# Kernel tuning notes

Measured on AMD Instinct MI355X. Metric: run time of the kernel, lower is better.

The kernel has to match this reference:

```python
import jax, jax.numpy as jnp
import numpy as np

IN, H1, H2, H3, H4, OUT = 512, 2048, 2048, 1024, 512, 1


def setup_inputs() -> dict:
    key = jax.random.key(0)
    ks = jax.random.split(key, 12)
    def lin(k, fan_in, fan_out):
        # torch Linear default init: U(-1/sqrt(fan_in), 1/sqrt(fan_in))
        bound = 1.0 / np.sqrt(fan_in)
        k1, k2 = jax.random.split(k)
        W = jax.random.uniform(k1, (fan_out, fan_in), jnp.float32, -bound, bound)
        b = jax.random.uniform(k2, (fan_out,), jnp.float32, -bound, bound)
        return W, b
    x = jax.random.normal(ks[0], (16384, IN), jnp.float32)
    cross_w = jnp.ones((IN,), jnp.float32)   # init.constant_(1.0)
    cross_b = jnp.zeros((IN,), jnp.float32)  # init.constant_(0.0)
    W1, b1 = lin(ks[1], IN, H1)
    W2, b2 = lin(ks[2], H1, H2)
    W3, b3 = lin(ks[3], H2, H3)
    W4, b4 = lin(ks[4], H3, H4)
    Wo, bo = lin(ks[5], H4, OUT)
    return {"x": x, "cross_w": cross_w, "cross_b": cross_b,
            "W1": W1, "b1": b1, "W2": W2, "b2": b2,
            "W3": W3, "b3": b3, "W4": W4, "b4": b4,
            "Wo": Wo, "bo": bo}


def reference(x, cross_w, cross_b, W1, b1, W2, b2, W3, b3, W4, b4, Wo, bo):
    # Cross layer: bmm(x0[...,None], x[...,None,:]) . w == x0 * (x . w)
    # (mathematically identical, avoids the O(f^2) outer product)
    xw = x @ cross_w                         # [B]
    h = x * xw[:, None] + cross_b + x        # [B, IN]
    h = jax.nn.relu(h @ W1.T + b1)           # [B, H1]
    h = jax.nn.relu(h @ W2.T + b2)           # [B, H2]
    h = jax.nn.relu(h @ W3.T + b3)           # [B, H3]
    h = jax.nn.relu(h @ W4.T + b4)           # [B, H4]
    return h @ Wo.T + bo                     # [B, OUT]
```

## Files before the change

kernel.cpp:

```cpp
#include <hip/hip_runtime.h>


#define BK 64

typedef __bf16 bf16x8 __attribute__((ext_vector_type(8)));
typedef float  f32x4  __attribute__((ext_vector_type(4)));
typedef unsigned short u16x4 __attribute__((ext_vector_type(4)));

__device__ __forceinline__ unsigned short f2bf(float f) {
    unsigned int u = __builtin_bit_cast(unsigned int, f);
    u += 0x7fffu + ((u >> 16) & 1u);
    return (unsigned short)(u >> 16);
}

__device__ __forceinline__ void async16(const void* g, void* l) {
    __builtin_amdgcn_global_load_lds(
        (const __attribute__((address_space(1))) unsigned int*)g,
        (__attribute__((address_space(3))) unsigned int*)l,
        16, 0, 0);
}

template<int BN>
__global__ __launch_bounds__(256, 2)
void gemm_bt_bias_relu(const unsigned short* __restrict__ A,
                       const unsigned short* __restrict__ B,
                       const float* __restrict__ bias,
                       unsigned short* __restrict__ C,
                       int M, int N, int K)
{
    constexpr int JT = BN / 32;
    __shared__ __align__(16) unsigned short As[128 * BK];
    __shared__ __align__(16) unsigned short Bs[BN * BK];

    const int tid  = threadIdx.x;
    const int lane = tid & 63;
    const int wave = tid >> 6;
    const int quad = lane >> 4;
    const int l16  = lane & 15;

    const int bm = blockIdx.x * 128;
    const int bn = blockIdx.y * BN;
    const int wm = (wave & 1) * 64;
    const int wn = (wave >> 1) * (BN / 2);

    const int lrow = tid >> 3;
    const int gcol = ((tid & 7) ^ (lrow & 7)) * 8;

    const unsigned short* gaBase = A + (size_t)(bm + lrow) * K + gcol;
    const unsigned short* gbBase = B + (size_t)(bn + lrow) * K + gcol;

    unsigned short* lA = As + tid * 8;
    unsigned short* lB = Bs + tid * 8;

    const int xa = l16 & 7;
    const unsigned short* As_w = As + (wm + l16) * BK;
    const unsigned short* Bs_w = Bs + (wn + l16) * BK;
    const int c0 = (quad ^ xa) * 8;
    const int c1 = ((quad ^ 4) ^ xa) * 8;

    f32x4 acc[4][JT] = {};

    for (int k0 = 0; k0 < K; k0 += BK) {
#pragma unroll
        for (int i = 0; i < 4; ++i)
            async16(gaBase + (size_t)(i * 32) * K + k0, lA + i * 2048);
#pragma unroll
        for (int i = 0; i < JT; ++i)
            async16(gbBase + (size_t)(i * 32) * K + k0, lB + i * 2048);
        __syncthreads();

#pragma unroll
        for (int kk = 0; kk < 2; ++kk) {
            const int cs = kk ? c1 : c0;
            bf16x8 af[4], bfr[JT];
#pragma unroll
            for (int i = 0; i < 4; ++i)  af[i]  = *(const bf16x8*)(As_w + i * 16 * BK + cs);
#pragma unroll
            for (int j = 0; j < JT; ++j) bfr[j] = *(const bf16x8*)(Bs_w + j * 16 * BK + cs);
#pragma unroll
            for (int i = 0; i < 4; ++i)
#pragma unroll
                for (int j = 0; j < JT; ++j)
                    acc[i][j] = __builtin_amdgcn_mfma_f32_16x16x32_bf16(
                        af[i], bfr[j], acc[i][j], 0, 0, 0);
        }
        __syncthreads();
    }

    float bv[JT];
#pragma unroll
    for (int j = 0; j < JT; ++j) bv[j] = bias[bn + wn + j * 16 + l16];

#pragma unroll
    for (int i = 0; i < 4; ++i) {
        const int row0 = bm + wm + i * 16 + quad * 4;
#pragma unroll
        for (int j = 0; j < JT; ++j) {
            const int col = bn + wn + j * 16 + l16;
#pragma unroll
            for (int r = 0; r < 4; ++r) {
                float v = acc[i][j][r] + bv[j];
                v = fmaxf(v, 0.0f);
                C[(size_t)(row0 + r) * N + col] = f2bf(v);
            }
        }
    }
}

__global__ __launch_bounds__(256, 2)
void gemm_bt_head(const unsigned short* __restrict__ A,
                  const unsigned short* __restrict__ B,
                  const float* __restrict__ bias,
                  const float* __restrict__ Wo,
                  float* __restrict__ out,
                  int M, int N, int K)
{
    constexpr int BN = 128;
    constexpr int JT = 4;
    __shared__ __align__(16) unsigned short As[128 * BK];
    __shared__ __align__(16) unsigned short Bs[BN * BK];

    const int tid  = threadIdx.x;
    const int lane = tid & 63;
    const int wave = tid >> 6;
    const int quad = lane >> 4;
    const int l16  = lane & 15;

    const int bm = blockIdx.x * 128;
    const int bn = blockIdx.y * BN;
    const int wm = (wave & 1) * 64;
    const int wn = (wave >> 1) * 64;

    const int lrow = tid >> 3;
    const int gcol = ((tid & 7) ^ (lrow & 7)) * 8;

    const unsigned short* gaBase = A + (size_t)(bm + lrow) * K + gcol;
    const unsigned short* gbBase = B + (size_t)(bn + lrow) * K + gcol;

    unsigned short* lA = As + tid * 8;
    unsigned short* lB = Bs + tid * 8;

    const int xa = l16 & 7;
    const unsigned short* As_w = As + (wm + l16) * BK;
    const unsigned short* Bs_w = Bs + (wn + l16) * BK;
    const int c0 = (quad ^ xa) * 8;
    const int c1 = ((quad ^ 4) ^ xa) * 8;

    f32x4 acc[4][JT] = {};

    for (int k0 = 0; k0 < K; k0 += BK) {
#pragma unroll
        for (int i = 0; i < 4; ++i)
            async16(gaBase + (size_t)(i * 32) * K + k0, lA + i * 2048);
#pragma unroll
        for (int i = 0; i < JT; ++i)
            async16(gbBase + (size_t)(i * 32) * K + k0, lB + i * 2048);
        __syncthreads();

#pragma unroll
        for (int kk = 0; kk < 2; ++kk) {
            const int cs = kk ? c1 : c0;
            bf16x8 af[4], bfr[JT];
#pragma unroll
            for (int i = 0; i < 4; ++i)  af[i]  = *(const bf16x8*)(As_w + i * 16 * BK + cs);
#pragma unroll
            for (int j = 0; j < JT; ++j) bfr[j] = *(const bf16x8*)(Bs_w + j * 16 * BK + cs);
#pragma unroll
            for (int i = 0; i < 4; ++i)
#pragma unroll
                for (int j = 0; j < JT; ++j)
                    acc[i][j] = __builtin_amdgcn_mfma_f32_16x16x32_bf16(
                        af[i], bfr[j], acc[i][j], 0, 0, 0);
        }
        __syncthreads();
    }

    float bv[JT], wov[JT];
#pragma unroll
    for (int j = 0; j < JT; ++j) {
        const int col = bn + wn + j * 16 + l16;
        bv[j]  = bias[col];
        wov[j] = Wo[col];
    }

#pragma unroll
    for (int i = 0; i < 4; ++i) {
#pragma unroll
        for (int r = 0; r < 4; ++r) {
            float ws = 0.f;
#pragma unroll
            for (int j = 0; j < JT; ++j) {
                float v = acc[i][j][r] + bv[j];
                v = fmaxf(v, 0.0f);
                ws += v * wov[j];
            }
#pragma unroll
            for (int off = 8; off > 0; off >>= 1)
                ws += __shfl_xor(ws, off, 64);
            if (l16 == 0) {
                const int row = bm + wm + i * 16 + quad * 4 + r;
                atomicAdd(&out[row], ws);
            }
        }
    }
}

__global__ __launch_bounds__(256)
void prep_kernel(const float* __restrict__ x, const float* __restrict__ cw,
                 const float* __restrict__ cb, unsigned short* __restrict__ h0,
                 const float* __restrict__ s1, const float* __restrict__ s2,
                 const float* __restrict__ s3, const float* __restrict__ s4,
                 unsigned short* __restrict__ d1, unsigned short* __restrict__ d2,
                 unsigned short* __restrict__ d3, unsigned short* __restrict__ d4,
                 const float* __restrict__ bo, float* __restrict__ out)
{
    const int b = blockIdx.x;
    if (b < 7680) {
        long t = (long)b * 256 + threadIdx.x;
        const float* s; unsigned short* d; long off;
        if (t < 262144L)       { s = s1; d = d1; off = t; }
        else if (t < 1310720L) { s = s2; d = d2; off = t - 262144L; }
        else if (t < 1835008L) { s = s3; d = d3; off = t - 1310720L; }
        else                   { s = s4; d = d4; off = t - 1835008L; }
        f32x4 f = *(const f32x4*)(s + off * 4);
        u16x4 o;
#pragma unroll
        for (int i = 0; i < 4; ++i) o[i] = f2bf(f[i]);
        *(u16x4*)(d + off * 4) = o;
    } else if (b < 11776) {
        const int row  = (b - 7680) * 4 + (threadIdx.x >> 6);
        const int lane = threadIdx.x & 63;
        const float* xr = x + (size_t)row * 512;
        float xv[8];
        float s = 0.f;
#pragma unroll
        for (int i = 0; i < 8; ++i) {
            const int c = lane + i * 64;
            xv[i] = xr[c];
            s += xv[i] * cw[c];
        }
#pragma unroll
        for (int off = 32; off > 0; off >>= 1) s += __shfl_down(s, off, 64);
        s = __shfl(s, 0, 64);
        unsigned short* hr = h0 + (size_t)row * 512;
#pragma unroll
        for (int i = 0; i < 8; ++i) {
            const int c = lane + i * 64;
            hr[c] = f2bf(xv[i] * s + cb[c] + xv[i]);
        }
    } else {
        const int t = (b - 11776) * 256 + threadIdx.x;
        out[t] = bo[0];
    }
}

extern "C" void kernel_launch(void* const* d_in, const int* in_sizes, int n_in,
                              void* d_out, int out_size, void* d_ws, size_t ws_size,
                              hipStream_t stream)
{
    const float* x  = (const float*)d_in[0];
    const float* cw = (const float*)d_in[1];
    const float* cb = (const float*)d_in[2];
    const float* W1 = (const float*)d_in[3];  const float* b1 = (const float*)d_in[4];
    const float* W2 = (const float*)d_in[5];  const float* b2 = (const float*)d_in[6];
    const float* W3 = (const float*)d_in[7];  const float* b3 = (const float*)d_in[8];
    const float* W4 = (const float*)d_in[9];  const float* b4 = (const float*)d_in[10];
    const float* Wo = (const float*)d_in[11]; const float* bo = (const float*)d_in[12];
    float* out = (float*)d_out;

    char* p = (char*)d_ws;
    unsigned short* wb1 = (unsigned short*)p; p += (size_t)2048 * 512  * 2;
    unsigned short* wb2 = (unsigned short*)p; p += (size_t)2048 * 2048 * 2;
    unsigned short* wb3 = (unsigned short*)p; p += (size_t)1024 * 2048 * 2;
    unsigned short* wb4 = (unsigned short*)p; p += (size_t)512  * 1024 * 2;
    unsigned short* actA = (unsigned short*)p; p += (size_t)16384 * 2048 * 2;
    unsigned short* actB = (unsigned short*)p;

    prep_kernel<<<11840, 256, 0, stream>>>(x, cw, cb, actA,
                                           W1, W2, W3, W4, wb1, wb2, wb3, wb4,
                                           bo, out);

    gemm_bt_bias_relu<256><<<dim3(128, 8), 256, 0, stream>>>(actA, wb1, b1, actB, 16384, 2048, 512);
    gemm_bt_bias_relu<256><<<dim3(128, 8), 256, 0, stream>>>(actB, wb2, b2, actA, 16384, 2048, 2048);
    gemm_bt_bias_relu<256><<<dim3(128, 4), 256, 0, stream>>>(actA, wb3, b3, actB, 16384, 1024, 2048);
    gemm_bt_head<<<dim3(128, 4), 256, 0, stream>>>(actB, wb4, b4, Wo, out, 16384, 512, 1024);
}
```

Baseline: 345.5 us.

## Warp-specialize GEMMs with producer waves and double-buffered LDS

Each GEMM block becomes 512 threads: four producer waves issue async global-to-LDS loads for the next K tile into a second buffer while four consumer waves run MFMAs on the current one. The intent is to hide global load latency behind compute and cut one barrier per K step. In exchange, LDS per block doubles, fewer blocks fit per CU, and half the waves do no math. Register pressure under the two-block launch bound may also cause spills.

New measurement: 384.8 us. 11.4% more time.

```diff
diff --git a/kernel.cpp b/kernel.cpp
--- a/kernel.cpp
+++ b/kernel.cpp
@@ -21,190 +21,231 @@
 }
 
 template<int BN>
-__global__ __launch_bounds__(256, 2)
-void gemm_bt_bias_relu(const unsigned short* __restrict__ A,
-                       const unsigned short* __restrict__ B,
-                       const float* __restrict__ bias,
-                       unsigned short* __restrict__ C,
-                       int M, int N, int K)
+__global__ __launch_bounds__(512, 2)
+void gemm_ws(const unsigned short* __restrict__ A,
+             const unsigned short* __restrict__ B,
+             const float* __restrict__ bias,
+             unsigned short* __restrict__ C,
+             int M, int N, int K)
 {
-    constexpr int JT = BN / 32;
-    __shared__ __align__(16) unsigned short As[128 * BK];
-    __shared__ __align__(16) unsigned short Bs[BN * BK];
+    constexpr int JT   = BN / 32;
+    constexpr int ABUF = 128 * BK;
+    constexpr int BBUF = BN * BK;
+    __shared__ __align__(16) unsigned short As[2 * ABUF];
+    __shared__ __align__(16) unsigned short Bs[2 * BBUF];
 
     const int tid  = threadIdx.x;
+    const int wave = tid >> 6;
     const int lane = tid & 63;
-    const int wave = tid >> 6;
+    const bool producer = wave < 4;
+
+    const int bm = blockIdx.x * 128;
+    const int bn = blockIdx.y * BN;
+    const int nk = K / BK;
+
+    const int lrow = (tid & 255) >> 3;
+    const int gcol = ((tid & 7) ^ (lrow & 7)) * 8;
+    const unsigned short* gaBase = A + (size_t)(bm + lrow) * K + gcol;
+    const unsigned short* gbBase = B + (size_t)(bn + lrow) * K + gcol;
+    unsigned short* lA = As + (tid & 255) * 8;
+    unsigned short* lB = Bs + (tid & 255) * 8;
+
+    const int cw   = wave - 4;
     const int quad = lane >> 4;
     const int l16  = lane & 15;
-
-    const int bm = blockIdx.x * 128;
-    const int bn = blockIdx.y * BN;
-    const int wm = (wave & 1) * 64;
-    const int wn = (wave >> 1) * (BN / 2);
-
-    const int lrow = tid >> 3;
-    const int gcol = ((tid & 7) ^ (lrow & 7)) * 8;
-
-    const unsigned short* gaBase = A + (size_t)(bm + lrow) * K + gcol;
-    const unsigned short* gbBase = B + (size_t)(bn + lrow) * K + gcol;
-
-    unsigned short* lA = As + tid * 8;
-    unsigned short* lB = Bs + tid * 8;
-
-    const int xa = l16 & 7;
-    const unsigned short* As_w = As + (wm + l16) * BK;
-    const unsigned short* Bs_w = Bs + (wn + l16) * BK;
-    const int c0 = (quad ^ xa) * 8;
-    const int c1 = ((quad ^ 4) ^ xa) * 8;
+    const int wm   = (cw & 1) * 64;
+    const int wn   = (cw >> 1) * (BN / 2);
+    const int xa   = l16 & 7;
+    const int c0   = (quad ^ xa) * 8;
+    const int c1   = ((quad ^ 4) ^ xa) * 8;
 
     f32x4 acc[4][JT] = {};
 
-    for (int k0 = 0; k0 < K; k0 += BK) {
+    if (producer) {
 #pragma unroll
         for (int i = 0; i < 4; ++i)
-            async16(gaBase + (size_t)(i * 32) * K + k0, lA + i * 2048);
+            async16(gaBase + (size_t)(i * 32) * K, lA + i * 2048);
 #pragma unroll
         for (int i = 0; i < JT; ++i)
-            async16(gbBase + (size_t)(i * 32) * K + k0, lB + i * 2048);
+            async16(gbBase + (size_t)(i * 32) * K, lB + i * 2048);
+    }
+    __syncthreads();
+
+    for (int k = 0; k < nk; ++k) {
+        if (producer) {
+            if (k + 1 < nk) {
+                const size_t ko = (size_t)(k + 1) * BK;
+                const int bo_ = (k + 1) & 1;
+#pragma unroll
+                for (int i = 0; i < 4; ++i)
+                    async16(gaBase + (size_t)(i * 32) * K + ko,
+                            lA + bo_ * ABUF + i * 2048);
+#pragma unroll
+                for (int i = 0; i < JT; ++i)
+                    async16(gbBase + (size_t)(i * 32) * K + ko,
+                            lB + bo_ * BBUF + i * 2048);
+            }
+        } else {
+            const unsigned short* As_w = As + (k & 1) * ABUF + (wm + l16) * BK;
+            const unsigned short* Bs_w = Bs + (k & 1) * BBUF + (wn + l16) * BK;
+#pragma unroll
+            for (int kk = 0; kk < 2; ++kk) {
+                const int cs = kk ? c1 : c0;
+                bf16x8 af[4], bfr[JT];
+#pragma unroll
+                for (int i = 0; i < 4; ++i)  af[i]  = *(const bf16x8*)(As_w + i * 16 * BK + cs);
+#pragma unroll
+                for (int j = 0; j < JT; ++j) bfr[j] = *(const bf16x8*)(Bs_w + j * 16 * BK + cs);
+#pragma unroll
+                for (int i = 0; i < 4; ++i)
+#pragma unroll
+                    for (int j = 0; j < JT; ++j)
+                        acc[i][j] = __builtin_amdgcn_mfma_f32_16x16x32_bf16(
+                            af[i], bfr[j], acc[i][j], 0, 0, 0);
+            }
+        }
         __syncthreads();
-
-#pragma unroll
-        for (int kk = 0; kk < 2; ++kk) {
-            const int cs = kk ? c1 : c0;
-            bf16x8 af[4], bfr[JT];
-#pragma unroll
-            for (int i = 0; i < 4; ++i)  af[i]  = *(const bf16x8*)(As_w + i * 16 * BK + cs);
-#pragma unroll
-            for (int j = 0; j < JT; ++j) bfr[j] = *(const bf16x8*)(Bs_w + j * 16 * BK + cs);
-#pragma unroll
-            for (int i = 0; i < 4; ++i)
-#pragma unroll
-                for (int j = 0; j < JT; ++j)
-                    acc[i][j] = __builtin_amdgcn_mfma_f32_16x16x32_bf16(
-                        af[i], bfr[j], acc[i][j], 0, 0, 0);
-        }
-        __syncthreads();
-    }
-
-    float bv[JT];
-#pragma unroll
-    for (int j = 0; j < JT; ++j) bv[j] = bias[bn + wn + j * 16 + l16];
-
-#pragma unroll
-    for (int i = 0; i < 4; ++i) {
-        const int row0 = bm + wm + i * 16 + quad * 4;
-#pragma unroll
-        for (int j = 0; j < JT; ++j) {
-            const int col = bn + wn + j * 16 + l16;
-#pragma unroll
-            for (int r = 0; r < 4; ++r) {
-                float v = acc[i][j][r] + bv[j];
-                v = fmaxf(v, 0.0f);
-                C[(size_t)(row0 + r) * N + col] = f2bf(v);
-            }
-        }
-    }
-}
-
-__global__ __launch_bounds__(256, 2)
-void gemm_bt_head(const unsigned short* __restrict__ A,
+    }
+
+    if (!producer) {
+        float bv[JT];
+#pragma unroll
+        for (int j = 0; j < JT; ++j) bv[j] = bias[bn + wn + j * 16 + l16];
+#pragma unroll
+        for (int i = 0; i < 4; ++i) {
+            const int row0 = bm + wm + i * 16 + quad * 4;
+#pragma unroll
+            for (int j = 0; j < JT; ++j) {
+                const int col = bn + wn + j * 16 + l16;
+#pragma unroll
+                for (int r = 0; r < 4; ++r) {
+                    float v = acc[i][j][r] + bv[j];
+                    v = fmaxf(v, 0.0f);
+                    C[(size_t)(row0 + r) * N + col] = f2bf(v);
+                }
+            }
+        }
+    }
+}
+
+__global__ __launch_bounds__(512, 2)
+void gemm_ws_head(const unsigned short* __restrict__ A,
                   const unsigned short* __restrict__ B,
                   const float* __restrict__ bias,
                   const float* __restrict__ Wo,
                   float* __restrict__ out,
                   int M, int N, int K)
 {
-    constexpr int BN = 128;
-    constexpr int JT = 4;
-    __shared__ __align__(16) unsigned short As[128 * BK];
-    __shared__ __align__(16) unsigned short Bs[BN * BK];
+    constexpr int BN = 128, JT = 4;
+    constexpr int ABUF = 128 * BK, BBUF = BN * BK;
+    __shared__ __align__(16) unsigned short As[2 * ABUF];
+    __shared__ __align__(16) unsigned short Bs[2 * BBUF];
 
     const int tid  = threadIdx.x;
+    const int wave = tid >> 6;
     const int lane = tid & 63;
-    const int wave = tid >> 6;
+    const bool producer = wave < 4;
+
+    const int bm = blockIdx.x * 128;
+    const int bn = blockIdx.y * BN;
+    const int nk = K / BK;
+
+    const int lrow = (tid & 255) >> 3;
+    const int gcol = ((tid & 7) ^ (lrow & 7)) * 8;
+    const unsigned short* gaBase = A + (size_t)(bm + lrow) * K + gcol;
+    const unsigned short* gbBase = B + (size_t)(bn + lrow) * K + gcol;
+    unsigned short* lA = As + (tid & 255) * 8;
+    unsigned short* lB = Bs + (tid & 255) * 8;
+
+    const int cw   = wave - 4;
     const int quad = lane >> 4;
     const int l16  = lane & 15;
-
-    const int bm = blockIdx.x * 128;
-    const int bn = blockIdx.y * BN;
-    const int wm = (wave & 1) * 64;
-    const int wn = (wave >> 1) * 64;
-
-    const int lrow = tid >> 3;
-    const int gcol = ((tid & 7) ^ (lrow & 7)) * 8;
-
-    const unsigned short* gaBase = A + (size_t)(bm + lrow) * K + gcol;
-    const unsigned short* gbBase = B + (size_t)(bn + lrow) * K + gcol;
-
-    unsigned short* lA = As + tid * 8;
-    unsigned short* lB = Bs + tid * 8;
-
-    const int xa = l16 & 7;
-    const unsigned short* As_w = As + (wm + l16) * BK;
-    const unsigned short* Bs_w = Bs + (wn + l16) * BK;
-    const int c0 = (quad ^ xa) * 8;
-    const int c1 = ((quad ^ 4) ^ xa) * 8;
+    const int wm   = (cw & 1) * 64;
+    const int wn   = (cw >> 1) * 64;
+    const int xa   = l16 & 7;
+    const int c0   = (quad ^ xa) * 8;
+    const int c1   = ((quad ^ 4) ^ xa) * 8;
 
     f32x4 acc[4][JT] = {};
 
-    for (int k0 = 0; k0 < K; k0 += BK) {
+    if (producer) {
 #pragma unroll
         for (int i = 0; i < 4; ++i)
-            async16(gaBase + (size_t)(i * 32) * K + k0, lA + i * 2048);
+            async16(gaBase + (size_t)(i * 32) * K, lA + i * 2048);
 #pragma unroll
         for (int i = 0; i < JT; ++i)
-            async16(gbBase + (size_t)(i * 32) * K + k0, lB + i * 2048);
+            async16(gbBase + (size_t)(i * 32) * K, lB + i * 2048);
+    }
+    __syncthreads();
+
+    for (int k = 0; k < nk; ++k) {
+        if (producer) {
+            if (k + 1 < nk) {
+                const size_t ko = (size_t)(k + 1) * BK;
+                const int bo_ = (k + 1) & 1;
+#pragma unroll
+                for (int i = 0; i < 4; ++i)
+                    async16(gaBase + (size_t)(i * 32) * K + ko,
+                            lA + bo_ * ABUF + i * 2048);
+#pragma unroll
+                for (int i = 0; i < JT; ++i)
+                    async16(gbBase + (size_t)(i * 32) * K + ko,
+                            lB + bo_ * BBUF + i * 2048);
+            }
+        } else {
+            const unsigned short* As_w = As + (k & 1) * ABUF + (wm + l16) * BK;
+            const unsigned short* Bs_w = Bs + (k & 1) * BBUF + (wn + l16) * BK;
+#pragma unroll
+            for (int kk = 0; kk < 2; ++kk) {
+                const int cs = kk ? c1 : c0;
+                bf16x8 af[4], bfr[JT];
+#pragma unroll
+                for (int i = 0; i < 4; ++i)  af[i]  = *(const bf16x8*)(As_w + i * 16 * BK + cs);
+#pragma unroll
+                for (int j = 0; j < JT; ++j) bfr[j] = *(const bf16x8*)(Bs_w + j * 16 * BK + cs);
+#pragma unroll
+                for (int i = 0; i < 4; ++i)
+#pragma unroll
+                    for (int j = 0; j < JT; ++j)
+                        acc[i][j] = __builtin_amdgcn_mfma_f32_16x16x32_bf16(
+                            af[i], bfr[j], acc[i][j], 0, 0, 0);
+            }
+        }
         __syncthreads();
-
-#pragma unroll
-        for (int kk = 0; kk < 2; ++kk) {
-            const int cs = kk ? c1 : c0;
-            bf16x8 af[4], bfr[JT];
-#pragma unroll
-            for (int i = 0; i < 4; ++i)  af[i]  = *(const bf16x8*)(As_w + i * 16 * BK + cs);
-#pragma unroll
-            for (int j = 0; j < JT; ++j) bfr[j] = *(const bf16x8*)(Bs_w + j * 16 * BK + cs);
-#pragma unroll
-            for (int i = 0; i < 4; ++i)
-#pragma unroll
-                for (int j = 0; j < JT; ++j)
-                    acc[i][j] = __builtin_amdgcn_mfma_f32_16x16x32_bf16(
-                        af[i], bfr[j], acc[i][j], 0, 0, 0);
-        }
-        __syncthreads();
-    }
-
-    float bv[JT], wov[JT];
-#pragma unroll
-    for (int j = 0; j < JT; ++j) {
-        const int col = bn + wn + j * 16 + l16;
-        bv[j]  = bias[col];
-        wov[j] = Wo[col];
-    }
-
-#pragma unroll
-    for (int i = 0; i < 4; ++i) {
-#pragma unroll
-        for (int r = 0; r < 4; ++r) {
-            float ws = 0.f;
-#pragma unroll
-            for (int j = 0; j < JT; ++j) {
-                float v = acc[i][j][r] + bv[j];
-                v = fmaxf(v, 0.0f);
-                ws += v * wov[j];
-            }
-#pragma unroll
-            for (int off = 8; off > 0; off >>= 1)
-                ws += __shfl_xor(ws, off, 64);
-            if (l16 == 0) {
-                const int row = bm + wm + i * 16 + quad * 4 + r;
-                atomicAdd(&out[row], ws);
-            }
-        }
-    }
-}
-
+    }
+
+    if (!producer) {
+        float bv[JT], wov[JT];
+#pragma unroll
+        for (int j = 0; j < JT; ++j) {
+            const int col = bn + wn + j * 16 + l16;
+            bv[j]  = bias[col];
+            wov[j] = Wo[col];
+        }
+#pragma unroll
+        for (int i = 0; i < 4; ++i) {
+#pragma unroll
+            for (int r = 0; r < 4; ++r) {
+                float ws = 0.f;
+#pragma unroll
+                for (int j = 0; j < JT; ++j) {
+                    float v = acc[i][j][r] + bv[j];
+                    v = fmaxf(v, 0.0f);
+                    ws += v * wov[j];
+                }
+#pragma unroll
+                for (int off = 8; off > 0; off >>= 1)
+                    ws += __shfl_xor(ws, off, 64);
+                if (l16 == 0) {
+                    const int row = bm + wm + i * 16 + quad * 4 + r;
+                    atomicAdd(&out[row], ws);
+                }
+            }
+        }
+    }
+}
+
+typedef float f32x4g __attribute__((ext_vector_type(4)));
 __global__ __launch_bounds__(256)
 void prep_kernel(const float* __restrict__ x, const float* __restrict__ cw,
                  const float* __restrict__ cb, unsigned short* __restrict__ h0,
@@ -222,7 +263,7 @@
         else if (t < 1310720L) { s = s2; d = d2; off = t - 262144L; }
         else if (t < 1835008L) { s = s3; d = d3; off = t - 1310720L; }
         else                   { s = s4; d = d4; off = t - 1835008L; }
-        f32x4 f = *(const f32x4*)(s + off * 4);
+        f32x4g f = *(const f32x4g*)(s + off * 4);
         u16x4 o;
 #pragma unroll
         for (int i = 0; i < 4; ++i) o[i] = f2bf(f[i]);
@@ -280,8 +321,8 @@
                                            W1, W2, W3, W4, wb1, wb2, wb3, wb4,
                                            bo, out);
 
-    gemm_bt_bias_relu<256><<<dim3(128, 8), 256, 0, stream>>>(actA, wb1, b1, actB, 16384, 2048, 512);
-    gemm_bt_bias_relu<256><<<dim3(128, 8), 256, 0, stream>>>(actB, wb2, b2, actA, 16384, 2048, 2048);
-    gemm_bt_bias_relu<256><<<dim3(128, 4), 256, 0, stream>>>(actA, wb3, b3, actB, 16384, 1024, 2048);
-    gemm_bt_head<<<dim3(128, 4), 256, 0, stream>>>(actB, wb4, b4, Wo, out, 16384, 512, 1024);
-}
+    gemm_ws<256><<<dim3(128, 8), 512, 0, stream>>>(actA, wb1, b1, actB, 16384, 2048, 512);
+    gemm_ws<256><<<dim3(128, 8), 512, 0, stream>>>(actB, wb2, b2, actA, 16384, 2048, 2048);
+    gemm_ws<256><<<dim3(128, 4), 512, 0, stream>>>(actA, wb3, b3, actB, 16384, 1024, 2048);
+    gemm_ws_head<<<dim3(128, 4), 512, 0, stream>>>(actB, wb4, b4, Wo, out, 16384, 512, 1024);
+}
```

## Overlap W2-W4 bf16 conversion with first GEMM in a combined launch

Applied to the files above, without the earlier changes.

Moves the fp32-to-bf16 conversion of W2, W3 and W4 out of the prep kernel into extra blocks of the first GEMM launch. Those conversion blocks can run alongside the layer-1 GEMM tiles and fill idle CUs instead of serialising before it. The prep kernel now only converts W1, computes the cross layer and initialises the output. The cost is a larger, mixed grid, and the GEMM tiles and conversion blocks compete for bandwidth.

Measured after the change: 353.7 us. 2.4% more time.

```diff
diff --git a/kernel.cpp b/kernel.cpp
--- a/kernel.cpp
+++ b/kernel.cpp
@@ -18,6 +18,92 @@
         (const __attribute__((address_space(1))) unsigned int*)g,
         (__attribute__((address_space(3))) unsigned int*)l,
         16, 0, 0);
+}
+
+template<int BN>
+__device__ __forceinline__ void gemm_body(const unsigned short* __restrict__ A,
+                                          const unsigned short* __restrict__ B,
+                                          const float* __restrict__ bias,
+                                          unsigned short* __restrict__ C,
+                                          int N, int K, int bx, int by)
+{
+    constexpr int JT = BN / 32;
+    __shared__ __align__(16) unsigned short As[128 * BK];
+    __shared__ __align__(16) unsigned short Bs[BN * BK];
+
+    const int tid  = threadIdx.x;
+    const int lane = tid & 63;
+    const int wave = tid >> 6;
+    const int quad = lane >> 4;
+    const int l16  = lane & 15;
+
+    const int bm = bx * 128;
+    const int bn = by * BN;
+    const int wm = (wave & 1) * 64;
+    const int wn = (wave >> 1) * (BN / 2);
+
+    const int lrow = tid >> 3;
+    const int gcol = ((tid & 7) ^ (lrow & 7)) * 8;
+
+    const unsigned short* gaBase = A + (size_t)(bm + lrow) * K + gcol;
+    const unsigned short* gbBase = B + (size_t)(bn + lrow) * K + gcol;
+
+    unsigned short* lA = As + tid * 8;
+    unsigned short* lB = Bs + tid * 8;
+
+    const int xa = l16 & 7;
+    const unsigned short* As_w = As + (wm + l16) * BK;
+    const unsigned short* Bs_w = Bs + (wn + l16) * BK;
+    const int c0 = (quad ^ xa) * 8;
+    const int c1 = ((quad ^ 4) ^ xa) * 8;
+
+    f32x4 acc[4][JT] = {};
+
+    for (int k0 = 0; k0 < K; k0 += BK) {
+#pragma unroll
+        for (int i = 0; i < 4; ++i)
+            async16(gaBase + (size_t)(i * 32) * K + k0, lA + i * 2048);
+#pragma unroll
+        for (int i = 0; i < JT; ++i)
+            async16(gbBase + (size_t)(i * 32) * K + k0, lB + i * 2048);
+        __syncthreads();
+
+#pragma unroll
+        for (int kk = 0; kk < 2; ++kk) {
+            const int cs = kk ? c1 : c0;
+            bf16x8 af[4], bfr[JT];
+#pragma unroll
+            for (int i = 0; i < 4; ++i)  af[i]  = *(const bf16x8*)(As_w + i * 16 * BK + cs);
+#pragma unroll
+            for (int j = 0; j < JT; ++j) bfr[j] = *(const bf16x8*)(Bs_w + j * 16 * BK + cs);
+#pragma unroll
+            for (int i = 0; i < 4; ++i)
+#pragma unroll
+                for (int j = 0; j < JT; ++j)
+                    acc[i][j] = __builtin_amdgcn_mfma_f32_16x16x32_bf16(
+                        af[i], bfr[j], acc[i][j], 0, 0, 0);
+        }
+        __syncthreads();
+    }
+
+    float bv[JT];
+#pragma unroll
+    for (int j = 0; j < JT; ++j) bv[j] = bias[bn + wn + j * 16 + l16];
+
+#pragma unroll
+    for (int i = 0; i < 4; ++i) {
+        const int row0 = bm + wm + i * 16 + quad * 4;
+#pragma unroll
+        for (int j = 0; j < JT; ++j) {
+            const int col = bn + wn + j * 16 + l16;
+#pragma unroll
+            for (int r = 0; r < 4; ++r) {
+                float v = acc[i][j][r] + bv[j];
+                v = fmaxf(v, 0.0f);
+                C[(size_t)(row0 + r) * N + col] = f2bf(v);
+            }
+        }
+    }
 }
 
 template<int BN>
@@ -26,84 +112,34 @@
                        const unsigned short* __restrict__ B,
                        const float* __restrict__ bias,
                        unsigned short* __restrict__ C,
-                       int M, int N, int K)
-{
-    constexpr int JT = BN / 32;
-    __shared__ __align__(16) unsigned short As[128 * BK];
-    __shared__ __align__(16) unsigned short Bs[BN * BK];
-
-    const int tid  = threadIdx.x;
-    const int lane = tid & 63;
-    const int wave = tid >> 6;
-    const int quad = lane >> 4;
-    const int l16  = lane & 15;
-
-    const int bm = blockIdx.x * 128;
-    const int bn = blockIdx.y * BN;
-    const int wm = (wave & 1) * 64;
-    const int wn = (wave >> 1) * (BN / 2);
-
-    const int lrow = tid >> 3;
-    const int gcol = ((tid & 7) ^ (lrow & 7)) * 8;
-
-    const unsigned short* gaBase = A + (size_t)(bm + lrow) * K + gcol;
-    const unsigned short* gbBase = B + (size_t)(bn + lrow) * K + gcol;
-
-    unsigned short* lA = As + tid * 8;
-    unsigned short* lB = Bs + tid * 8;
-
-    const int xa = l16 & 7;
-    const unsigned short* As_w = As + (wm + l16) * BK;
-    const unsigned short* Bs_w = Bs + (wn + l16) * BK;
-    const int c0 = (quad ^ xa) * 8;
-    const int c1 = ((quad ^ 4) ^ xa) * 8;
-
-    f32x4 acc[4][JT] = {};
-
-    for (int k0 = 0; k0 < K; k0 += BK) {
-#pragma unroll
-        for (int i = 0; i < 4; ++i)
-            async16(gaBase + (size_t)(i * 32) * K + k0, lA + i * 2048);
-#pragma unroll
-        for (int i = 0; i < JT; ++i)
-            async16(gbBase + (size_t)(i * 32) * K + k0, lB + i * 2048);
-        __syncthreads();
-
-#pragma unroll
-        for (int kk = 0; kk < 2; ++kk) {
-            const int cs = kk ? c1 : c0;
-            bf16x8 af[4], bfr[JT];
-#pragma unroll
-            for (int i = 0; i < 4; ++i)  af[i]  = *(const bf16x8*)(As_w + i * 16 * BK + cs);
-#pragma unroll
-            for (int j = 0; j < JT; ++j) bfr[j] = *(const bf16x8*)(Bs_w + j * 16 * BK + cs);
-#pragma unroll
-            for (int i = 0; i < 4; ++i)
-#pragma unroll
-                for (int j = 0; j < JT; ++j)
-                    acc[i][j] = __builtin_amdgcn_mfma_f32_16x16x32_bf16(
-                        af[i], bfr[j], acc[i][j], 0, 0, 0);
-        }
-        __syncthreads();
-    }
-
-    float bv[JT];
-#pragma unroll
-    for (int j = 0; j < JT; ++j) bv[j] = bias[bn + wn + j * 16 + l16];
-
-#pragma unroll
-    for (int i = 0; i < 4; ++i) {
-        const int row0 = bm + wm + i * 16 + quad * 4;
-#pragma unroll
-        for (int j = 0; j < JT; ++j) {
-            const int col = bn + wn + j * 16 + l16;
-#pragma unroll
-            for (int r = 0; r < 4; ++r) {
-                float v = acc[i][j][r] + bv[j];
-                v = fmaxf(v, 0.0f);
-                C[(size_t)(row0 + r) * N + col] = f2bf(v);
-            }
-        }
+                       int N, int K)
+{
+    gemm_body<BN>(A, B, bias, C, N, K, blockIdx.x, blockIdx.y);
+}
+
+__global__ __launch_bounds__(256, 2)
+void gemm1_conv(const unsigned short* __restrict__ A,
+                const unsigned short* __restrict__ B,
+                const float* __restrict__ bias,
+                unsigned short* __restrict__ C,
+                const float* __restrict__ s2, const float* __restrict__ s3,
+                const float* __restrict__ s4,
+                unsigned short* __restrict__ d2, unsigned short* __restrict__ d3,
+                unsigned short* __restrict__ d4)
+{
+    if (blockIdx.x < 128) {
+        gemm_body<256>(A, B, bias, C, 2048, 512, blockIdx.x, blockIdx.y);
+    } else {
+        long t = ((long)(blockIdx.x - 128) * 8 + blockIdx.y) * 256 + threadIdx.x;
+        const float* s; unsigned short* d; long off;
+        if (t < 1048576L)      { s = s2; d = d2; off = t; }
+        else if (t < 1572864L) { s = s3; d = d3; off = t - 1048576L; }
+        else                   { s = s4; d = d4; off = t - 1572864L; }
+        f32x4 f = *(const f32x4*)(s + off * 4);
+        u16x4 o;
+#pragma unroll
+        for (int i = 0; i < 4; ++i) o[i] = f2bf(f[i]);
+        *(u16x4*)(d + off * 4) = o;
     }
 }
 
@@ -113,10 +149,9 @@
                   const float* __restrict__ bias,
                   const float* __restrict__ Wo,
                   float* __restrict__ out,
-                  int M, int N, int K)
-{
-    constexpr int BN = 128;
-    constexpr int JT = 4;
+                  int N, int K)
+{
+    constexpr int BN = 128, JT = 4;
     __shared__ __align__(16) unsigned short As[128 * BK];
     __shared__ __align__(16) unsigned short Bs[BN * BK];
 
@@ -208,27 +243,12 @@
 __global__ __launch_bounds__(256)
 void prep_kernel(const float* __restrict__ x, const float* __restrict__ cw,
                  const float* __restrict__ cb, unsigned short* __restrict__ h0,
-                 const float* __restrict__ s1, const float* __restrict__ s2,
-                 const float* __restrict__ s3, const float* __restrict__ s4,
-                 unsigned short* __restrict__ d1, unsigned short* __restrict__ d2,
-                 unsigned short* __restrict__ d3, unsigned short* __restrict__ d4,
+                 const float* __restrict__ s1, unsigned short* __restrict__ d1,
                  const float* __restrict__ bo, float* __restrict__ out)
 {
     const int b = blockIdx.x;
-    if (b < 7680) {
-        long t = (long)b * 256 + threadIdx.x;
-        const float* s; unsigned short* d; long off;
-        if (t < 262144L)       { s = s1; d = d1; off = t; }
-        else if (t < 1310720L) { s = s2; d = d2; off = t - 262144L; }
-        else if (t < 1835008L) { s = s3; d = d3; off = t - 1310720L; }
-        else                   { s = s4; d = d4; off = t - 1835008L; }
-        f32x4 f = *(const f32x4*)(s + off * 4);
-        u16x4 o;
-#pragma unroll
-        for (int i = 0; i < 4; ++i) o[i] = f2bf(f[i]);
-        *(u16x4*)(d + off * 4) = o;
-    } else if (b < 11776) {
-        const int row  = (b - 7680) * 4 + (threadIdx.x >> 6);
+    if (b < 4096) {
+        const int row  = b * 4 + (threadIdx.x >> 6);
         const int lane = threadIdx.x & 63;
         const float* xr = x + (size_t)row * 512;
         float xv[8];
@@ -248,8 +268,15 @@
             const int c = lane + i * 64;
             hr[c] = f2bf(xv[i] * s + cb[c] + xv[i]);
         }
+    } else if (b < 5120) {
+        long off = (long)(b - 4096) * 256 + threadIdx.x;
+        f32x4 f = *(const f32x4*)(s1 + off * 4);
+        u16x4 o;
+#pragma unroll
+        for (int i = 0; i < 4; ++i) o[i] = f2bf(f[i]);
+        *(u16x4*)(d1 + off * 4) = o;
     } else {
-        const int t = (b - 11776) * 256 + threadIdx.x;
+        const int t = (b - 5120) * 256 + threadIdx.x;
         out[t] = bo[0];
     }
 }
@@ -276,12 +303,11 @@
     unsigned short* actA = (unsigned short*)p; p += (size_t)16384 * 2048 * 2;
     unsigned short* actB = (unsigned short*)p;
 
-    prep_kernel<<<11840, 256, 0, stream>>>(x, cw, cb, actA,
-                                           W1, W2, W3, W4, wb1, wb2, wb3, wb4,
-                                           bo, out);
-
-    gemm_bt_bias_relu<256><<<dim3(128, 8), 256, 0, stream>>>(actA, wb1, b1, actB, 16384, 2048, 512);
-    gemm_bt_bias_relu<256><<<dim3(128, 8), 256, 0, stream>>>(actB, wb2, b2, actA, 16384, 2048, 2048);
-    gemm_bt_bias_relu<256><<<dim3(128, 4), 256, 0, stream>>>(actA, wb3, b3, actB, 16384, 1024, 2048);
-    gemm_bt_head<<<dim3(128, 4), 256, 0, stream>>>(actB, wb4, b4, Wo, out, 16384, 512, 1024);
-}
+    prep_kernel<<<5184, 256, 0, stream>>>(x, cw, cb, actA, W1, wb1, bo, out);
+
+    gemm1_conv<<<dim3(960, 8), 256, 0, stream>>>(actA, wb1, b1, actB,
+                                                 W2, W3, W4, wb2, wb3, wb4);
+    gemm_bt_bias_relu<256><<<dim3(128, 8), 256, 0, stream>>>(actB, wb2, b2, actA, 2048, 2048);
+    gemm_bt_bias_relu<256><<<dim3(128, 4), 256, 0, stream>>>(actA, wb3, b3, actB, 1024, 2048);
+    gemm_bt_head<<<dim3(128, 4), 256, 0, stream>>>(actB, wb4, b4, Wo, out, 512, 1024);
+}
```

## Load A fragments directly from global into registers with prefetch, drop A LDS tile

Applied to the files above, without the earlier changes.

The A operand no longer goes through LDS. Each wave loads its own MFMA A fragments straight from global memory into registers, and the next K-step's fragments are prefetched into a second register set while the current step computes. The goal is to cut LDS traffic and shared-memory footprint for A and to overlap A loads with MFMA work. The costs are more registers, uncoalesced 16-byte-per-lane global loads, and duplicated A reads across the two waves that share the same rows.

New measurement: 447.8 us. 1.3x slower.

```diff
diff --git a/kernel.cpp b/kernel.cpp
--- a/kernel.cpp
+++ b/kernel.cpp
@@ -26,10 +26,9 @@
                        const unsigned short* __restrict__ B,
                        const float* __restrict__ bias,
                        unsigned short* __restrict__ C,
-                       int M, int N, int K)
+                       int N, int K)
 {
     constexpr int JT = BN / 32;
-    __shared__ __align__(16) unsigned short As[128 * BK];
     __shared__ __align__(16) unsigned short Bs[BN * BK];
 
     const int tid  = threadIdx.x;
@@ -45,36 +44,48 @@
 
     const int lrow = tid >> 3;
     const int gcol = ((tid & 7) ^ (lrow & 7)) * 8;
-
-    const unsigned short* gaBase = A + (size_t)(bm + lrow) * K + gcol;
     const unsigned short* gbBase = B + (size_t)(bn + lrow) * K + gcol;
-
-    unsigned short* lA = As + tid * 8;
     unsigned short* lB = Bs + tid * 8;
 
     const int xa = l16 & 7;
-    const unsigned short* As_w = As + (wm + l16) * BK;
     const unsigned short* Bs_w = Bs + (wn + l16) * BK;
     const int c0 = (quad ^ xa) * 8;
     const int c1 = ((quad ^ 4) ^ xa) * 8;
 
+    const unsigned short* gA[4];
+#pragma unroll
+    for (int i = 0; i < 4; ++i)
+        gA[i] = A + (size_t)(bm + wm + i * 16 + l16) * K + quad * 8;
+
     f32x4 acc[4][JT] = {};
-
-    for (int k0 = 0; k0 < K; k0 += BK) {
-#pragma unroll
-        for (int i = 0; i < 4; ++i)
-            async16(gaBase + (size_t)(i * 32) * K + k0, lA + i * 2048);
+    bf16x8 afc[4][2], afn[4][2];
+
+#pragma unroll
+    for (int i = 0; i < 4; ++i)
+#pragma unroll
+        for (int kk = 0; kk < 2; ++kk)
+            afc[i][kk] = *(const bf16x8*)(gA[i] + kk * 32);
+
+    const int nk = K / BK;
+    for (int k = 0; k < nk; ++k) {
+        const int k0 = k * BK;
 #pragma unroll
         for (int i = 0; i < JT; ++i)
             async16(gbBase + (size_t)(i * 32) * K + k0, lB + i * 2048);
         __syncthreads();
 
+        if (k + 1 < nk) {
+#pragma unroll
+            for (int i = 0; i < 4; ++i)
+#pragma unroll
+                for (int kk = 0; kk < 2; ++kk)
+                    afn[i][kk] = *(const bf16x8*)(gA[i] + k0 + BK + kk * 32);
+        }
+
 #pragma unroll
         for (int kk = 0; kk < 2; ++kk) {
             const int cs = kk ? c1 : c0;
-            bf16x8 af[4], bfr[JT];
-#pragma unroll
-            for (int i = 0; i < 4; ++i)  af[i]  = *(const bf16x8*)(As_w + i * 16 * BK + cs);
+            bf16x8 bfr[JT];
 #pragma unroll
             for (int j = 0; j < JT; ++j) bfr[j] = *(const bf16x8*)(Bs_w + j * 16 * BK + cs);
 #pragma unroll
@@ -82,9 +93,14 @@
 #pragma unroll
                 for (int j = 0; j < JT; ++j)
                     acc[i][j] = __builtin_amdgcn_mfma_f32_16x16x32_bf16(
-                        af[i], bfr[j], acc[i][j], 0, 0, 0);
+                        afc[i][kk], bfr[j], acc[i][j], 0, 0, 0);
         }
         __syncthreads();
+#pragma unroll
+        for (int i = 0; i < 4; ++i)
+#pragma unroll
+            for (int kk = 0; kk < 2; ++kk)
+                afc[i][kk] = afn[i][kk];
     }
 
     float bv[JT];
@@ -113,11 +129,9 @@
                   const float* __restrict__ bias,
                   const float* __restrict__ Wo,
                   float* __restrict__ out,
-                  int M, int N, int K)
+                  int N, int K)
 {
-    constexpr int BN = 128;
-    constexpr int JT = 4;
-    __shared__ __align__(16) unsigned short As[128 * BK];
+    constexpr int BN = 128, JT = 4;
     __shared__ __align__(16) unsigned short Bs[BN * BK];
 
     const int tid  = threadIdx.x;
@@ -133,36 +147,47 @@
 
     const int lrow = tid >> 3;
     const int gcol = ((tid & 7) ^ (lrow & 7)) * 8;
-
-    const unsigned short* gaBase = A + (size_t)(bm + lrow) * K + gcol;
     const unsigned short* gbBase = B + (size_t)(bn + lrow) * K + gcol;
-
-    unsigned short* lA = As + tid * 8;
     unsigned short* lB = Bs + tid * 8;
 
     const int xa = l16 & 7;
-    const unsigned short* As_w = As + (wm + l16) * BK;
     const unsigned short* Bs_w = Bs + (wn + l16) * BK;
     const int c0 = (quad ^ xa) * 8;
     const int c1 = ((quad ^ 4) ^ xa) * 8;
 
+    const unsigned short* gA[4];
+#pragma unroll
+    for (int i = 0; i < 4; ++i)
+        gA[i] = A + (size_t)(bm + wm + i * 16 + l16) * K + quad * 8;
+
     f32x4 acc[4][JT] = {};
-
-    for (int k0 = 0; k0 < K; k0 += BK) {
-#pragma unroll
-        for (int i = 0; i < 4; ++i)
-            async16(gaBase + (size_t)(i * 32) * K + k0, lA + i * 2048);
+    bf16x8 afc[4][2], afn[4][2];
+#pragma unroll
+    for (int i = 0; i < 4; ++i)
+#pragma unroll
+        for (int kk = 0; kk < 2; ++kk)
+            afc[i][kk] = *(const bf16x8*)(gA[i] + kk * 32);
+
+    const int nk = K / BK;
+    for (int k = 0; k < nk; ++k) {
+        const int k0 = k * BK;
 #pragma unroll
         for (int i = 0; i < JT; ++i)
             async16(gbBase + (size_t)(i * 32) * K + k0, lB + i * 2048);
         __syncthreads();
 
+        if (k + 1 < nk) {
+#pragma unroll
+            for (int i = 0; i < 4; ++i)
+#pragma unroll
+                for (int kk = 0; kk < 2; ++kk)
+                    afn[i][kk] = *(const bf16x8*)(gA[i] + k0 + BK + kk * 32);
+        }
+
 #pragma unroll
         for (int kk = 0; kk < 2; ++kk) {
             const int cs = kk ? c1 : c0;
-            bf16x8 af[4], bfr[JT];
-#pragma unroll
-            for (int i = 0; i < 4; ++i)  af[i]  = *(const bf16x8*)(As_w + i * 16 * BK + cs);
+            bf16x8 bfr[JT];
 #pragma unroll
             for (int j = 0; j < JT; ++j) bfr[j] = *(const bf16x8*)(Bs_w + j * 16 * BK + cs);
 #pragma unroll
@@ -170,9 +195,14 @@
 #pragma unroll
                 for (int j = 0; j < JT; ++j)
                     acc[i][j] = __builtin_amdgcn_mfma_f32_16x16x32_bf16(
-                        af[i], bfr[j], acc[i][j], 0, 0, 0);
+                        afc[i][kk], bfr[j], acc[i][j], 0, 0, 0);
         }
         __syncthreads();
+#pragma unroll
+        for (int i = 0; i < 4; ++i)
+#pragma unroll
+            for (int kk = 0; kk < 2; ++kk)
+                afc[i][kk] = afn[i][kk];
     }
 
     float bv[JT], wov[JT];
@@ -280,8 +310,8 @@
                                            W1, W2, W3, W4, wb1, wb2, wb3, wb4,
                                            bo, out);
 
-    gemm_bt_bias_relu<256><<<dim3(128, 8), 256, 0, stream>>>(actA, wb1, b1, actB, 16384, 2048, 512);
-    gemm_bt_bias_relu<256><<<dim3(128, 8), 256, 0, stream>>>(actB, wb2, b2, actA, 16384, 2048, 2048);
-    gemm_bt_bias_relu<256><<<dim3(128, 4), 256, 0, stream>>>(actA, wb3, b3, actB, 16384, 1024, 2048);
-    gemm_bt_head<<<dim3(128, 4), 256, 0, stream>>>(actB, wb4, b4, Wo, out, 16384, 512, 1024);
-}
+    gemm_bt_bias_relu<256><<<dim3(128, 8), 256, 0, stream>>>(actA, wb1, b1, actB, 2048, 512);
+    gemm_bt_bias_relu<256><<<dim3(128, 8), 256, 0, stream>>>(actB, wb2, b2, actA, 2048, 2048);
+    gemm_bt_bias_relu<256><<<dim3(128, 4), 256, 0, stream>>>(actA, wb3, b3, actB, 1024, 2048);
+    gemm_bt_head<<<dim3(128, 4), 256, 0, stream>>>(actB, wb4, b4, Wo, out, 512, 1024);
+}
```
